# Optimization experiments

Measured on AMD Instinct MI355X. Metric: run time of the kernel, lower is better.

## Reference

```python
import jax, jax.numpy as jnp
import numpy as np

B, S, E, H, F, V = 4, 2048, 1024, 16, 4096, 32000
D = E // H  # head_dim = 64
LN_EPS = 1e-5


def layer_norm(x, g, b):
    mu = jnp.mean(x, axis=-1, keepdims=True)
    var = jnp.mean(jnp.square(x - mu), axis=-1, keepdims=True)
    return (x - mu) * jax.lax.rsqrt(var + LN_EPS) * g + b


def setup_inputs() -> dict:
    key = jax.random.key(0)
    ks = jax.random.split(key, 12)
    s = 0.02
    return {
        "input_ids": jax.random.randint(ks[0], (B, S), 0, V),
        "attention_mask": jnp.ones((B, S), dtype=jnp.int32),
        "emb_table": jax.random.normal(ks[1], (V, E), jnp.float32) * s,
        "Wq": jax.random.normal(ks[2], (E, E), jnp.float32) * s,
        "bq": jnp.zeros((E,), jnp.float32),
        "Wk": jax.random.normal(ks[3], (E, E), jnp.float32) * s,
        "bk": jnp.zeros((E,), jnp.float32),
        "Wv": jax.random.normal(ks[4], (E, E), jnp.float32) * s,
        "bv": jnp.zeros((E,), jnp.float32),
        "Wo": jax.random.normal(ks[5], (E, E), jnp.float32) * s,
        "bo": jnp.zeros((E,), jnp.float32),
        "ln_g": jnp.ones((E,), jnp.float32),
        "ln_b": jnp.zeros((E,), jnp.float32),
        "W1": jax.random.normal(ks[6], (E, F), jnp.float32) * s,
        "b1": jnp.zeros((F,), jnp.float32),
        "W2": jax.random.normal(ks[7], (F, E), jnp.float32) * s,
        "b2": jnp.zeros((E,), jnp.float32),
        "Wp": jax.random.normal(ks[8], (E, 3), jnp.float32) * s,
        "bp": jnp.zeros((3,), jnp.float32),
    }


def reference(input_ids, attention_mask, emb_table, Wq, bq, Wk, bk, Wv, bv,
              Wo, bo, ln_g, ln_b, W1, b1, W2, b2, Wp, bp):
    b, s = input_ids.shape
    x = emb_table[input_ids]                                  # [B,S,E]
    q = (x @ Wq + bq).reshape(b, s, H, D).transpose(0, 2, 1, 3)  # [B,H,S,D]
    k = (x @ Wk + bk).reshape(b, s, H, D).transpose(0, 2, 1, 3)
    v = (x @ Wv + bv).reshape(b, s, H, D).transpose(0, 2, 1, 3)
    scores = jnp.einsum('bhqd,bhkd->bhqk', q, k) / jnp.sqrt(jnp.float32(D))
    mask = attention_mask[:, None, None, :]                   # [B,1,1,S]
    scores = jnp.where(mask == 0, -jnp.inf, scores)
    attn = jax.nn.softmax(scores, axis=-1)
    ctx = jnp.einsum('bhqk,bhkd->bhqd', attn, v)              # [B,H,S,D]
    ctx = ctx.transpose(0, 2, 1, 3).reshape(b, s, E)
    ctx = ctx @ Wo + bo
    h = layer_norm(ctx + x, ln_g, ln_b)
    ff = jax.nn.gelu(h @ W1 + b1, approximate=False) @ W2 + b2
    logits = ff @ Wp + bp                                     # [B,S,3]
    return logits.mean(axis=1)                                # [B,3]
```

## Files before the change

### kernel.cpp

```cpp
#include <hip/hip_runtime.h>
#include <hip/hip_bf16.h>
#include <math.h>

#define BB 4
#define SS 2048
#define EE 1024
#define HH 16
#define DD 64
#define FF 4096

typedef unsigned short u16;
typedef unsigned int u32;
typedef __bf16 bf16x8 __attribute__((ext_vector_type(8)));
typedef float f32x4 __attribute__((ext_vector_type(4)));

static __device__ __forceinline__ float gelu_exact(float v){
  return 0.5f * v * (1.0f + erff(v * 0.70710678118654752f));
}

static __device__ __forceinline__ u16 f2bf(float f){
  union { float f; u32 u; } x; x.f = f;
  u32 r = x.u + 0x7FFFu + ((x.u >> 16) & 1u);
  return (u16)(r >> 16);
}
static __device__ __forceinline__ u16 f2bf_hw(float f){
  union { __bf16 b; u16 u; } c; c.b = (__bf16)f; return c.u;
}
static __device__ __forceinline__ void unpack2(u32 u, float& lo, float& hi){
  union { u32 u; float f; } a, b;
  a.u = u << 16; b.u = u & 0xFFFF0000u;
  lo = a.f; hi = b.f;
}

#define GLOAD_LDS16(g, l) \
  __builtin_amdgcn_global_load_lds((const __attribute__((address_space(1))) void*)(g), \
      (__attribute__((address_space(3))) void*)(l), 16, 0, 0)

static __device__ __forceinline__ void blockbar(){
  asm volatile("" ::: "memory");
  __builtin_amdgcn_s_barrier();
  asm volatile("" ::: "memory");
}

__global__ __launch_bounds__(256) void embed_kernel(const int* __restrict__ ids,
    const float* __restrict__ emb, float* __restrict__ xf, u16* __restrict__ xbf){
  int row = blockIdx.x;
  int id  = ids[row];
  float4 v = ((const float4*)(emb + (size_t)id * EE))[threadIdx.x];
  ((float4*)(xf + (size_t)row * EE))[threadIdx.x] = v;
  ushort4 u; u.x = f2bf(v.x); u.y = f2bf(v.y); u.z = f2bf(v.z); u.w = f2bf(v.w);
  ((ushort4*)(xbf + (size_t)row * EE))[threadIdx.x] = u;
}

__global__ __launch_bounds__(256) void mask_prep(const int* __restrict__ mask,
    float* __restrict__ mbias){
  int i = blockIdx.x * 256 + threadIdx.x;
  mbias[i] = (mask[i] != 0) ? 0.f : -1e30f;
}

__global__ __launch_bounds__(256) void prep_weights(const float* __restrict__ Wq,
    const float* __restrict__ Wk, const float* __restrict__ Wv,
    const float* __restrict__ Wo, const float* __restrict__ W1, u16* __restrict__ WT){
  __shared__ float tile[32][33];
  int bid = blockIdx.x;
  const float* W; u16* dst; int N, n0, k0;
  if (bid < 4096){
    W = W1; dst = WT + (size_t)4 * EE * EE; N = FF;
    n0 = (bid & 127) * 32; k0 = (bid >> 7) * 32;
  } else {
    int idx = bid - 4096;
    int which = idx >> 10, t = idx & 1023;
    W = (which == 0) ? Wq : (which == 1) ? Wk : (which == 2) ? Wv : Wo;
    dst = WT + (size_t)which * EE * EE; N = EE;
    n0 = (t & 31) * 32; k0 = (t >> 5) * 32;
  }
  int tx = threadIdx.x & 31, ty = threadIdx.x >> 5;
  #pragma unroll
  for (int i = 0; i < 4; i++)
    tile[ty + 8*i][tx] = W[(size_t)(k0 + ty + 8*i) * N + n0 + tx];
  __syncthreads();
  #pragma unroll
  for (int i = 0; i < 4; i++)
    dst[(size_t)(n0 + ty + 8*i) * EE + k0 + tx] = f2bf(tile[tx][ty + 8*i]);
}

template<int MODE>
__global__ __launch_bounds__(256) void gemm_mfma(const u16* __restrict__ A,
    const u16* __restrict__ WT, const float* __restrict__ bias,
    const float* __restrict__ biasB, const float* __restrict__ biasC,
    u16* __restrict__ C, float* __restrict__ gsum, int M, int N, int K){
  __shared__ __attribute__((aligned(16))) u16 As[2][128 * 32];
  __shared__ __attribute__((aligned(16))) u16 Bs[2][128 * 32];

  const int tid = threadIdx.x;
  const int l = tid & 63, w = tid >> 6;
  const int lm = l & 15, lq = l >> 4;
  const int wm = (w >> 1) * 64, wn = (w & 1) * 64;

  const int nwg = gridDim.x * gridDim.y;
  const int bid = blockIdx.y * gridDim.x + blockIdx.x;
  const int q8  = nwg >> 3;
  const int lin = (bid & 7) * q8 + (bid >> 3);
  const int bx  = lin % gridDim.x;
  const int by  = lin / gridDim.x;
  const int r0 = by * 128, c0 = bx * 128;

  const int srow0 = w * 32 + (l >> 2);
  const int scol  = (l & 3) * 8;
  const u16* Ab = A  + (size_t)(r0 + srow0) * K + scol;
  const u16* Bb = WT + (size_t)(c0 + srow0) * K + scol;
  const int sbase = (w * 2) * 512;

  f32x4 acc[4][4];
  const f32x4 zero = {0.f, 0.f, 0.f, 0.f};
  #pragma unroll
  for (int mi = 0; mi < 4; mi++)
    #pragma unroll
    for (int ni = 0; ni < 4; ni++) acc[mi][ni] = zero;

  GLOAD_LDS16(Ab,                  &As[0][sbase]);
  GLOAD_LDS16(Ab + (size_t)16 * K, &As[0][sbase + 512]);
  GLOAD_LDS16(Bb,                  &Bs[0][sbase]);
  GLOAD_LDS16(Bb + (size_t)16 * K, &Bs[0][sbase + 512]);
  __syncthreads();

  int p = 0;
  for (int k0 = 0; k0 < K; k0 += 32){
    if (k0 + 32 < K){
      const int pn = p ^ 1;
      GLOAD_LDS16(Ab + k0 + 32,                   &As[pn][sbase]);
      GLOAD_LDS16(Ab + (size_t)16 * K + k0 + 32,  &As[pn][sbase + 512]);
      GLOAD_LDS16(Bb + k0 + 32,                   &Bs[pn][sbase]);
      GLOAD_LDS16(Bb + (size_t)16 * K + k0 + 32,  &Bs[pn][sbase + 512]);
    }
    bf16x8 af[4], bfr[4];
    #pragma unroll
    for (int mi = 0; mi < 4; mi++)
      af[mi] = *(const bf16x8*)&As[p][(wm + mi*16 + lm) * 32 + lq * 8];
    #pragma unroll
    for (int ni = 0; ni < 4; ni++)
      bfr[ni] = *(const bf16x8*)&Bs[p][(wn + ni*16 + lm) * 32 + lq * 8];
    #pragma unroll
    for (int mi = 0; mi < 4; mi++)
      #pragma unroll
      for (int ni = 0; ni < 4; ni++)
        acc[mi][ni] = __builtin_amdgcn_mfma_f32_16x16x32_bf16(af[mi], bfr[ni], acc[mi][ni], 0, 0, 0);
    __syncthreads();
    p ^= 1;
  }

  if constexpr (MODE == 0){
    #pragma unroll
    for (int ni = 0; ni < 4; ni++){
      int col = c0 + wn + ni*16 + lm;
      float bcol = bias[col];
      #pragma unroll
      for (int mi = 0; mi < 4; mi++){
        #pragma unroll
        for (int r = 0; r < 4; r++){
          int row = r0 + wm + mi*16 + lq*4 + r;
          C[(size_t)row * N + col] = f2bf(acc[mi][ni][r] + bcol);
        }
      }
    }
  }
}

template<int MODE>
__global__ __launch_bounds__(512, 2) void gemm256(const u16* __restrict__ A,
    const u16* __restrict__ WT, const float* __restrict__ bias,
    const float* __restrict__ biasB, const float* __restrict__ biasC,
    u16* __restrict__ C, float* __restrict__ gsum, int M, int N, int K){
  __shared__ __attribute__((aligned(16))) u16 As[2 * 256 * 64];
  __shared__ __attribute__((aligned(16))) u16 Bs[2 * 256 * 64];

  const int tid = threadIdx.x;
  const int w = tid >> 6, l = tid & 63;
  const int lm = l & 15, lq = l >> 4;
  const int wm = (w >> 2) * 128, wn = (w & 3) * 64;

  const int nwg = gridDim.x * gridDim.y;
  const int bid = blockIdx.y * gridDim.x + blockIdx.x;
  const int lin = (bid & 7) * (nwg >> 3) + (bid >> 3);
  const int bx = lin % gridDim.x, by = lin / gridDim.x;
  const int r0 = by * 256, c0 = bx * 256;

  const int NT = K >> 6;
  const int arow = w * 8 + (l >> 3);
  const int acol = ((l & 7) ^ (l >> 3)) * 8;
  const u16* Ag = A  + (size_t)(r0 + arow) * K + acol;
  const u16* Bg = WT + (size_t)(c0 + arow) * K + acol;
  const int dstw = w * 512;

#define STG_A(p_, kt_, g_) GLOAD_LDS16(Ag + (size_t)((g_)*64) * K + (kt_)*64, &As[(p_)*16384 + (g_)*4096 + dstw])
#define STG_B(p_, kt_, g_) GLOAD_LDS16(Bg + (size_t)((g_)*64) * K + (kt_)*64, &Bs[(p_)*16384 + (g_)*4096 + dstw])

  const int rsw = (lm & 7) << 3;
#define RD_A(p_, mi_, kk_) (*(const bf16x8*)&As[(p_)*16384 + (wm + (mi_)*16 + lm)*64 + (((kk_)*32 + lq*8) ^ rsw)])
#define RD_B(p_, ni_, kk_) (*(const bf16x8*)&Bs[(p_)*16384 + (wn + (ni_)*16 + lm)*64 + (((kk_)*32 + lq*8) ^ rsw)])

  f32x4 acc[8][4];
  const f32x4 zero = {0.f, 0.f, 0.f, 0.f};
  #pragma unroll
  for (int mi = 0; mi < 8; mi++)
    #pragma unroll
    for (int ni = 0; ni < 4; ni++) acc[mi][ni] = zero;

  #pragma unroll
  for (int g = 0; g < 4; g++){ STG_A(0, 0, g); STG_B(0, 0, g); }
  #pragma unroll
  for (int g = 0; g < 4; g++){ STG_A(1, 1, g); STG_B(1, 1, g); }
  asm volatile("s_waitcnt vmcnt(8)" ::: "memory");
  __builtin_amdgcn_s_barrier();
  asm volatile("" ::: "memory");

  bf16x8 a0[4][2], a1[4][2], b0[2][2], b1[2][2];

  for (int t = 0; t < NT; ++t){
    const int p = t & 1;
    const int s = t + 2;
    const bool st = (s < NT);

    #pragma unroll
    for (int mi = 0; mi < 4; mi++){ a0[mi][0] = RD_A(p, mi, 0); a0[mi][1] = RD_A(p, mi, 1); }
    #pragma unroll
    for (int ni = 0; ni < 2; ni++){ b0[ni][0] = RD_B(p, ni, 0); b0[ni][1] = RD_B(p, ni, 1); }
    blockbar();
    __builtin_amdgcn_s_setprio(1);
    #pragma unroll
    for (int kk = 0; kk < 2; kk++)
      #pragma unroll
      for (int mi = 0; mi < 4; mi++)
        #pragma unroll
        for (int ni = 0; ni < 2; ni++)
          acc[mi][ni] = __builtin_amdgcn_mfma_f32_16x16x32_bf16(a0[mi][kk], b0[ni][kk], acc[mi][ni], 0, 0, 0);
    __builtin_amdgcn_s_setprio(0);
    blockbar();

    #pragma unroll
    for (int ni = 0; ni < 2; ni++){ b1[ni][0] = RD_B(p, ni + 2, 0); b1[ni][1] = RD_B(p, ni + 2, 1); }
    if (st){ STG_A(p, s, 0); STG_A(p, s, 2); }
    blockbar();
    __builtin_amdgcn_s_setprio(1);
    #pragma unroll
    for (int kk = 0; kk < 2; kk++)
      #pragma unroll
      for (int mi = 0; mi < 4; mi++)
        #pragma unroll
        for (int ni = 0; ni < 2; ni++)
          acc[mi][ni + 2] = __builtin_amdgcn_mfma_f32_16x16x32_bf16(a0[mi][kk], b1[ni][kk], acc[mi][ni + 2], 0, 0, 0);
    __builtin_amdgcn_s_setprio(0);
    blockbar();

    #pragma unroll
    for (int mi = 0; mi < 4; mi++){ a1[mi][0] = RD_A(p, mi + 4, 0); a1[mi][1] = RD_A(p, mi + 4, 1); }
    if (st){ STG_B(p, s, 0); STG_B(p, s, 1); }
    blockbar();
    __builtin_amdgcn_s_setprio(1);
    #pragma unroll
    for (int kk = 0; kk < 2; kk++)
      #pragma unroll
      for (int mi = 0; mi < 4; mi++)
        #pragma unroll
        for (int ni = 0; ni < 2; ni++)
          acc[mi + 4][ni] = __builtin_amdgcn_mfma_f32_16x16x32_bf16(a1[mi][kk], b0[ni][kk], acc[mi + 4][ni], 0, 0, 0);
    __builtin_amdgcn_s_setprio(0);
    blockbar();

    if (st){ STG_A(p, s, 1); STG_A(p, s, 3); STG_B(p, s, 2); STG_B(p, s, 3); }
    blockbar();
    __builtin_amdgcn_s_setprio(1);
    #pragma unroll
    for (int kk = 0; kk < 2; kk++)
      #pragma unroll
      for (int mi = 0; mi < 4; mi++)
        #pragma unroll
        for (int ni = 0; ni < 2; ni++)
          acc[mi + 4][ni + 2] = __builtin_amdgcn_mfma_f32_16x16x32_bf16(a1[mi][kk], b1[ni][kk], acc[mi + 4][ni + 2], 0, 0, 0);
    __builtin_amdgcn_s_setprio(0);
    if (t + 1 < NT){
      if (st) asm volatile("s_waitcnt vmcnt(8)" ::: "memory");
      else    asm volatile("s_waitcnt vmcnt(0)" ::: "memory");
      __builtin_amdgcn_s_barrier();
      asm volatile("" ::: "memory");
    }
  }

#undef STG_A
#undef STG_B
#undef RD_A
#undef RD_B

  if constexpr (MODE == 2){
    #pragma unroll
    for (int ni = 0; ni < 4; ni++){
      int col3 = c0 + wn + ni*16 + lm;
      int sel  = col3 >> 10;
      int colm = col3 & 1023;
      const float* bp_ = (sel == 0) ? bias : ((sel == 1) ? biasB : biasC);
      float bcol = bp_[colm];
      u16* dst = C + (size_t)sel * ((size_t)M * 1024);
      #pragma unroll
      for (int mi = 0; mi < 8; mi++){
        #pragma unroll
        for (int r = 0; r < 4; r++){
          int row = r0 + wm + mi*16 + lq*4 + r;
          dst[(size_t)row * 1024 + colm] = f2bf(acc[mi][ni][r] + bcol);
        }
      }
    }
  } else {
    const int batch = (r0 + wm) >> 11;
    #pragma unroll
    for (int ni = 0; ni < 4; ni++){
      int col = c0 + wn + ni*16 + lm;
      float bcol = bias[col];
      float cs = 0.f;
      #pragma unroll
      for (int mi = 0; mi < 8; mi++)
        #pragma unroll
        for (int r = 0; r < 4; r++)
          cs += gelu_exact(acc[mi][ni][r] + bcol);
      cs += __shfl_xor(cs, 16, 64);
      cs += __shfl_xor(cs, 32, 64);
      if (lq == 0) atomicAdd(&gsum[(size_t)batch * N + col], cs);
    }
  }
}

__global__ __launch_bounds__(256, 2) void attn_mfma(const u16* __restrict__ q,
    const u16* __restrict__ k, const u16* __restrict__ v,
    const float* __restrict__ mbias, u16* __restrict__ ctx){
  const int bid = blockIdx.y * gridDim.x + blockIdx.x;
  const int lin = (bid & 7) * 128 + (bid >> 3);
  const int qb  = lin & 15, bh = lin >> 4;
  const int b = bh >> 4, h = bh & 15;
  const int q0 = qb * 128;
  const int tid = threadIdx.x;
  const int w = tid >> 6, l = tid & 63, lm = l & 15, lq = l >> 4;

  __shared__ __attribute__((aligned(16))) u16 smem[128 * 72];
  u16* Kt = smem;
  u16* Vt = smem + 64 * 72;

  bf16x8 aq[2][2];
  #pragma unroll
  for (int mg = 0; mg < 2; mg++){
    const u16* qrow = q + (size_t)(b*SS + q0 + w*32 + mg*16 + lm) * EE + h*DD + lq*8;
    aq[mg][0] = *(const bf16x8*)qrow;
    aq[mg][1] = *(const bf16x8*)(qrow + 32);
  }

  f32x4 occ[2][4];
  const f32x4 zero = {0.f,0.f,0.f,0.f};
  #pragma unroll
  for (int mg = 0; mg < 2; mg++)
    #pragma unroll
    for (int mi = 0; mi < 4; mi++) occ[mg][mi] = zero;
  float l_part[2] = {0.f, 0.f};

  const int kkey = tid >> 2, kc16 = (tid & 3) * 16;
  const u16* kbase = k + (size_t)(b*SS + kkey) * EE + h*DD + kc16;
  const int kp = tid & 31, vd0 = (tid >> 5) * 8;
  const int vslot = ((kp >> 1) & 3) * 8 + ((kp >> 3) & 1) * 4 + (kp & 1) * 2 + (kp >> 4) * 32;
  const u16* vbase0 = v + (size_t)(b*SS + 2*kp) * EE + h*DD + vd0;
  const u16* vbase1 = vbase0 + EE;

  uint4 kr0 = *(const uint4*)(kbase);
  uint4 kr1 = *(const uint4*)(kbase + 8);
  uint4 vr0 = *(const uint4*)(vbase0);
  uint4 vr1 = *(const uint4*)(vbase1);

  const float SCALE_LOG2E = 0.125f * 1.4426950408889634f;
  const float* mrow = mbias + (size_t)b * SS;

  for (int t0 = 0; t0 < SS; t0 += 64){
    *(uint4*)&Kt[kkey*72 + kc16]     = kr0;
    *(uint4*)&Kt[kkey*72 + kc16 + 8] = kr1;
    {
      union { uint4 u; u16 s[8]; } va, vb;
      va.u = vr0; vb.u = vr1;
      #pragma unroll
      for (int i = 0; i < 8; i++){
        u32 pk = (u32)va.s[i] | ((u32)vb.s[i] << 16);
        *(u32*)&Vt[(vd0 + i)*72 + vslot] = pk;
      }
    }
    __syncthreads();

    if (t0 + 64 < SS){
      kr0 = *(const uint4*)(kbase + (size_t)(t0 + 64) * EE);
      kr1 = *(const uint4*)(kbase + (size_t)(t0 + 64) * EE + 8);
      vr0 = *(const uint4*)(vbase0 + (size_t)(t0 + 64) * EE);
      vr1 = *(const uint4*)(vbase1 + (size_t)(t0 + 64) * EE);
    }

    f32x4 mt[4];
    #pragma unroll
    for (int ni = 0; ni < 4; ni++)
      mt[ni] = *(const f32x4*)&mrow[t0 + ni*16 + lq*4];

    bf16x8 pb[2][2];
    #pragma unroll
    for (int mg = 0; mg < 2; mg++){
      float lp = 0.f;
      #pragma unroll
      for (int h2 = 0; h2 < 2; h2++){
        u32 pk_[2][2];
        #pragma unroll
        for (int np = 0; np < 2; np++){
          int ni = h2*2 + np;
          bf16x8 kf0 = *(const bf16x8*)&Kt[(ni*16 + lm)*72 + lq*8];
          bf16x8 kf1 = *(const bf16x8*)&Kt[(ni*16 + lm)*72 + 32 + lq*8];
          f32x4 sc = zero;
          __builtin_amdgcn_s_setprio(1);
          sc = __builtin_amdgcn_mfma_f32_16x16x32_bf16(kf0, aq[mg][0], sc, 0, 0, 0);
          sc = __builtin_amdgcn_mfma_f32_16x16x32_bf16(kf1, aq[mg][1], sc, 0, 0, 0);
          __builtin_amdgcn_s_setprio(0);
          float p[4];
          #pragma unroll
          for (int r = 0; r < 4; r++){
            float s = fminf(fmaf(sc[r], SCALE_LOG2E, mt[ni][r]), 80.f);
            p[r] = __builtin_amdgcn_exp2f(s);
            lp += p[r];
          }
          pk_[np][0] = (u32)f2bf_hw(p[0]) | ((u32)f2bf_hw(p[1]) << 16);
          pk_[np][1] = (u32)f2bf_hw(p[2]) | ((u32)f2bf_hw(p[3]) << 16);
        }
        union { u32 u[4]; bf16x8 v; } pu;
        pu.u[0] = pk_[0][0];
        pu.u[1] = pk_[0][1];
        pu.u[2] = pk_[1][0];
        pu.u[3] = pk_[1][1];
        pb[mg][h2] = pu.v;
      }
      l_part[mg] += lp;
    }

    __builtin_amdgcn_s_setprio(1);
    #pragma unroll
    for (int mi = 0; mi < 4; mi++){
      bf16x8 vb0 = *(const bf16x8*)&Vt[(mi*16 + lm)*72 + lq*8];
      bf16x8 vb1 = *(const bf16x8*)&Vt[(mi*16 + lm)*72 + 32 + lq*8];
      #pragma unroll
      for (int mg = 0; mg < 2; mg++){
        occ[mg][mi] = __builtin_amdgcn_mfma_f32_16x16x32_bf16(vb0, pb[mg][0], occ[mg][mi], 0, 0, 0);
        occ[mg][mi] = __builtin_amdgcn_mfma_f32_16x16x32_bf16(vb1, pb[mg][1], occ[mg][mi], 0, 0, 0);
      }
    }
    __builtin_amdgcn_s_setprio(0);
    __syncthreads();
  }

  #pragma unroll
  for (int mg = 0; mg < 2; mg++){
    float s = l_part[mg];
    s += __shfl_xor(s, 16, 64);
    s += __shfl_xor(s, 32, 64);
    float inv = 1.f / s;
    #pragma unroll
    for (int mi = 0; mi < 4; mi++){
      ushort4 o;
      o.x = f2bf(occ[mg][mi][0] * inv);
      o.y = f2bf(occ[mg][mi][1] * inv);
      o.z = f2bf(occ[mg][mi][2] * inv);
      o.w = f2bf(occ[mg][mi][3] * inv);
      *(ushort4*)&smem[(w*32 + mg*16 + lm)*72 + mi*16 + lq*4] = o;
    }
  }
  __syncthreads();
  {
    const int row = tid >> 1, half = tid & 1;
    u16* dst = ctx + (size_t)(b*SS + q0 + row) * EE + h*DD + half*32;
    const u16* src = &smem[row*72 + half*32];
    #pragma unroll
    for (int jj = 0; jj < 4; jj++)
      *(uint4*)(dst + jj*8) = *(const uint4*)(src + jj*8);
  }
}

__global__ __launch_bounds__(256) void ln_kernel(const u16* __restrict__ c2,
    const float* __restrict__ x, const float* __restrict__ g,
    const float* __restrict__ bta, u16* __restrict__ h){
  int row = blockIdx.x, tid = threadIdx.x;
  uint2 cu = ((const uint2*)(c2 + (size_t)row * EE))[tid];
  float c0,c1,c2f,c3;
  unpack2(cu.x, c0, c1); unpack2(cu.y, c2f, c3);
  float4 xv = ((const float4*)(x + (size_t)row * EE))[tid];
  float4 y = make_float4(c0+xv.x, c1+xv.y, c2f+xv.z, c3+xv.w);
  float s  = y.x + y.y + y.z + y.w;
  float ss = y.x*y.x + y.y*y.y + y.z*y.z + y.w*y.w;
  #pragma unroll
  for (int off=32; off; off>>=1){
    s  += __shfl_xor(s,  off, 64);
    ss += __shfl_xor(ss, off, 64);
  }
  __shared__ float rs[4], rss[4];
  int w = tid >> 6;
  if ((tid & 63) == 0){ rs[w] = s; rss[w] = ss; }
  __syncthreads();
  float tot  = rs[0]+rs[1]+rs[2]+rs[3];
  float tots = rss[0]+rss[1]+rss[2]+rss[3];
  float mu  = tot  * (1.f/EE);
  float var = tots * (1.f/EE) - mu*mu;
  float inv = rsqrtf(var + 1e-5f);
  float4 gv = ((const float4*)g)[tid];
  float4 bv = ((const float4*)bta)[tid];
  ushort4 ou;
  ou.x = f2bf((y.x-mu)*inv*gv.x + bv.x);
  ou.y = f2bf((y.y-mu)*inv*gv.y + bv.y);
  ou.z = f2bf((y.z-mu)*inv*gv.z + bv.z);
  ou.w = f2bf((y.w-mu)*inv*gv.w + bv.w);
  ((ushort4*)(h + (size_t)row * EE))[tid] = ou;
}

__global__ __launch_bounds__(256) void w2wp_kernel(const float* __restrict__ W2,
    const float* __restrict__ Wp, float* __restrict__ W2Wp){
  int f0 = blockIdx.x * 8;
  int tid = threadIdx.x;
  int e0 = tid * 4;
  float wp[4][3];
  #pragma unroll
  for (int t = 0; t < 4; t++)
    #pragma unroll
    for (int j = 0; j < 3; j++) wp[t][j] = Wp[(e0 + t)*3 + j];
  __shared__ float red[3][4];
  for (int i = 0; i < 8; i++){
    int f = f0 + i;
    float4 wv = ((const float4*)(W2 + (size_t)f * EE))[tid];
    float w4[4] = {wv.x, wv.y, wv.z, wv.w};
    float p[3] = {0.f, 0.f, 0.f};
    #pragma unroll
    for (int t = 0; t < 4; t++)
      #pragma unroll
      for (int j = 0; j < 3; j++) p[j] += w4[t] * wp[t][j];
    #pragma unroll
    for (int j = 0; j < 3; j++){
      float sj = p[j];
      #pragma unroll
      for (int off = 32; off; off >>= 1) sj += __shfl_xor(sj, off, 64);
      if ((tid & 63) == 0) red[j][tid >> 6] = sj;
    }
    __syncthreads();
    if (tid < 3) W2Wp[f*3 + tid] = red[tid][0] + red[tid][1] + red[tid][2] + red[tid][3];
    __syncthreads();
  }
}

__global__ __launch_bounds__(256) void out_final(const float* __restrict__ gsum,
    const float* __restrict__ W2Wp, const float* __restrict__ b2,
    const float* __restrict__ Wp, const float* __restrict__ bp, float* __restrict__ out){
  int tid = threadIdx.x;
  float part[4][3];
  #pragma unroll
  for (int b = 0; b < 4; b++)
    #pragma unroll
    for (int j = 0; j < 3; j++) part[b][j] = 0.f;
  for (int f = tid; f < FF; f += 256){
    float w0 = W2Wp[f*3], w1 = W2Wp[f*3+1], w2v = W2Wp[f*3+2];
    #pragma unroll
    for (int b = 0; b < 4; b++){
      float g = gsum[b*FF + f] * (1.f/SS);
      part[b][0] += g * w0; part[b][1] += g * w1; part[b][2] += g * w2v;
    }
  }
  float bb[3] = {0.f, 0.f, 0.f};
  for (int e = tid; e < EE; e += 256){
    float bv = b2[e];
    bb[0] += bv * Wp[e*3]; bb[1] += bv * Wp[e*3+1]; bb[2] += bv * Wp[e*3+2];
  }
  __shared__ float red[15][4];
  int lane = tid & 63, w = tid >> 6;
  #pragma unroll
  for (int b = 0; b < 4; b++)
    #pragma unroll
    for (int j = 0; j < 3; j++){
      float s = part[b][j];
      #pragma unroll
      for (int off = 32; off; off >>= 1) s += __shfl_xor(s, off, 64);
      if (lane == 0) red[b*3 + j][w] = s;
    }
  #pragma unroll
  for (int j = 0; j < 3; j++){
    float s = bb[j];
    #pragma unroll
    for (int off = 32; off; off >>= 1) s += __shfl_xor(s, off, 64);
    if (lane == 0) red[12 + j][w] = s;
  }
  __syncthreads();
  if (tid < 12){
    int j = tid % 3;
    float s  = red[tid][0] + red[tid][1] + red[tid][2] + red[tid][3];
    float bj = red[12+j][0] + red[12+j][1] + red[12+j][2] + red[12+j][3];
    out[tid] = s + bj + bp[j];
  }
}

extern "C" void kernel_launch(void* const* d_in, const int* in_sizes, int n_in,
                              void* d_out, int out_size, void* d_ws, size_t ws_size,
                              hipStream_t stream) {
  const int M = BB * SS;
  const int* ids  = (const int*)d_in[0];
  const int* mask = (const int*)d_in[1];
  const float* emb = (const float*)d_in[2];
  const float* Wq = (const float*)d_in[3];  const float* bq = (const float*)d_in[4];
  const float* Wk = (const float*)d_in[5];  const float* bk = (const float*)d_in[6];
  const float* Wv = (const float*)d_in[7];  const float* bv = (const float*)d_in[8];
  const float* Wo = (const float*)d_in[9];  const float* bo = (const float*)d_in[10];
  const float* lg = (const float*)d_in[11]; const float* lb = (const float*)d_in[12];
  const float* W1 = (const float*)d_in[13]; const float* b1 = (const float*)d_in[14];
  const float* W2 = (const float*)d_in[15]; const float* b2 = (const float*)d_in[16];
  const float* Wp = (const float*)d_in[17]; const float* bp = (const float*)d_in[18];

  char* base = (char*)d_ws;
  const size_t SLOTF = (size_t)M * EE;
  float* xf   = (float*)base;
  u16*  xbf   = (u16*)(base + SLOTF*4);
  u16*  qbf   = (u16*)(base + SLOTF*6);
  u16*  kbf   = (u16*)(base + SLOTF*8);
  u16*  vbf   = (u16*)(base + SLOTF*10);
  u16*  ctxbf = (u16*)(base + SLOTF*12);
  u16*  c2bf  = qbf;
  u16*  hbf   = kbf;
  u16*  WqT   = (u16*)(base + SLOTF*14);
  u16*  W1T   = WqT + (size_t)4*EE*EE;
  float* gsum = (float*)(W1T + (size_t)FF*EE);
  float* w2wp = gsum + BB*FF;
  float* mbias = w2wp + FF*3;

  hipMemsetAsync(gsum, 0, BB*FF*sizeof(float), stream);

  embed_kernel<<<M, 256, 0, stream>>>(ids, emb, xf, xbf);
  mask_prep<<<BB*SS/256, 256, 0, stream>>>(mask, mbias);

  prep_weights<<<8192, 256, 0, stream>>>(Wq, Wk, Wv, Wo, W1, WqT);
  w2wp_kernel<<<FF/8, 256, 0, stream>>>(W2, Wp, w2wp);

  gemm256<2><<<dim3(3*EE/256, M/256), 512, 0, stream>>>(
      xbf, WqT, bq, bk, bv, qbf, nullptr, M, EE, EE);

  attn_mfma<<<dim3(SS/128, BB*HH), 256, 0, stream>>>(qbf, kbf, vbf, mbias, ctxbf);

  gemm_mfma<0><<<dim3(EE/128, M/128), 256, 0, stream>>>(
      ctxbf, WqT + (size_t)3*EE*EE, bo, nullptr, nullptr, c2bf, nullptr, M, EE, EE);

  ln_kernel<<<M, 256, 0, stream>>>(c2bf, xf, lg, lb, hbf);

  gemm256<1><<<dim3(FF/256, M/256), 512, 0, stream>>>(
      hbf, W1T, b1, nullptr, nullptr, nullptr, gsum, M, FF, EE);

  out_final<<<1, 256, 0, stream>>>(gsum, w2wp, b2, Wp, bp, (float*)d_out);
}
```

Measured before the change: 593.5 us.

## Stream K tiles directly to LDS with double-buffered swizzled layout in attention

The attention kernel now loads K tiles with direct global-to-LDS loads (GLOAD_LDS16) into two ping-pong buffers with an XOR swizzle instead of padded rows staged through registers. This removes the register round trip and the LDS store instructions for K, and lets the next tile's K load overlap with the current compute. It also drops the fminf clamp before exp2, which saves an instruction per score but removes overflow protection. Shared memory grows from 128*72 to 12800 elements, which could affect occupancy.

```diff
diff --git a/kernel.cpp b/kernel.cpp
--- a/kernel.cpp
+++ b/kernel.cpp
@@ -339,9 +339,10 @@
   const int tid = threadIdx.x;
   const int w = tid >> 6, l = tid & 63, lm = l & 15, lq = l >> 4;
 
-  __shared__ __attribute__((aligned(16))) u16 smem[128 * 72];
-  u16* Kt = smem;
-  u16* Vt = smem + 64 * 72;
+  __shared__ __attribute__((aligned(16))) u16 smem[12800];
+  u16* Kt0 = smem;
+  u16* Kt1 = smem + 4096;
+  u16* Vt  = smem + 8192;
 
   bf16x8 aq[2][2];
   #pragma unroll
@@ -359,24 +360,29 @@
     for (int mi = 0; mi < 4; mi++) occ[mg][mi] = zero;
   float l_part[2] = {0.f, 0.f};
 
-  const int kkey = tid >> 2, kc16 = (tid & 3) * 16;
-  const u16* kbase = k + (size_t)(b*SS + kkey) * EE + h*DD + kc16;
+  const int krow = (l >> 3);
+  const int kchk = ((l & 7) ^ (krow & 7)) * 8;
+  const u16* kg0 = k + (size_t)(b*SS + w*16 + krow) * EE + h*DD + kchk;
+  const u16* kg1 = kg0 + (size_t)8 * EE;
+  const int kd0 = w*1024;
+  const int kd1 = w*1024 + 512;
+  const int rswl = (lm & 7) << 3;
+
   const int kp = tid & 31, vd0 = (tid >> 5) * 8;
   const int vslot = ((kp >> 1) & 3) * 8 + ((kp >> 3) & 1) * 4 + (kp & 1) * 2 + (kp >> 4) * 32;
   const u16* vbase0 = v + (size_t)(b*SS + 2*kp) * EE + h*DD + vd0;
   const u16* vbase1 = vbase0 + EE;
 
-  uint4 kr0 = *(const uint4*)(kbase);
-  uint4 kr1 = *(const uint4*)(kbase + 8);
+  GLOAD_LDS16(kg0, &Kt0[kd0]);
+  GLOAD_LDS16(kg1, &Kt0[kd1]);
   uint4 vr0 = *(const uint4*)(vbase0);
   uint4 vr1 = *(const uint4*)(vbase1);
 
   const float SCALE_LOG2E = 0.125f * 1.4426950408889634f;
   const float* mrow = mbias + (size_t)b * SS;
 
+  int p = 0;
   for (int t0 = 0; t0 < SS; t0 += 64){
-    *(uint4*)&Kt[kkey*72 + kc16]     = kr0;
-    *(uint4*)&Kt[kkey*72 + kc16 + 8] = kr1;
     {
       union { uint4 u; u16 s[8]; } va, vb;
       va.u = vr0; vb.u = vr1;
@@ -389,11 +395,13 @@
     __syncthreads();
 
     if (t0 + 64 < SS){
-      kr0 = *(const uint4*)(kbase + (size_t)(t0 + 64) * EE);
-      kr1 = *(const uint4*)(kbase + (size_t)(t0 + 64) * EE + 8);
+      u16* Ktn = p ? Kt0 : Kt1;
+      GLOAD_LDS16(kg0 + (size_t)(t0 + 64) * EE, &Ktn[kd0]);
+      GLOAD_LDS16(kg1 + (size_t)(t0 + 64) * EE, &Ktn[kd1]);
       vr0 = *(const uint4*)(vbase0 + (size_t)(t0 + 64) * EE);
       vr1 = *(const uint4*)(vbase1 + (size_t)(t0 + 64) * EE);
     }
+    const u16* Ktp = p ? Kt1 : Kt0;
 
     f32x4 mt[4];
     #pragma unroll
@@ -410,22 +418,22 @@
         #pragma unroll
         for (int np = 0; np < 2; np++){
           int ni = h2*2 + np;
-          bf16x8 kf0 = *(const bf16x8*)&Kt[(ni*16 + lm)*72 + lq*8];
-          bf16x8 kf1 = *(const bf16x8*)&Kt[(ni*16 + lm)*72 + 32 + lq*8];
+          bf16x8 kf0 = *(const bf16x8*)&Ktp[(ni*16 + lm)*64 + ((lq*8) ^ rswl)];
+          bf16x8 kf1 = *(const bf16x8*)&Ktp[(ni*16 + lm)*64 + ((32 + lq*8) ^ rswl)];
           f32x4 sc = zero;
           __builtin_amdgcn_s_setprio(1);
           sc = __builtin_amdgcn_mfma_f32_16x16x32_bf16(kf0, aq[mg][0], sc, 0, 0, 0);
           sc = __builtin_amdgcn_mfma_f32_16x16x32_bf16(kf1, aq[mg][1], sc, 0, 0, 0);
           __builtin_amdgcn_s_setprio(0);
-          float p[4];
+          float pr[4];
           #pragma unroll
           for (int r = 0; r < 4; r++){
-            float s = fminf(fmaf(sc[r], SCALE_LOG2E, mt[ni][r]), 80.f);
-            p[r] = __builtin_amdgcn_exp2f(s);
-            lp += p[r];
+            float s = fmaf(sc[r], SCALE_LOG2E, mt[ni][r]);
+            pr[r] = __builtin_amdgcn_exp2f(s);
+            lp += pr[r];
           }
-          pk_[np][0] = (u32)f2bf_hw(p[0]) | ((u32)f2bf_hw(p[1]) << 16);
-          pk_[np][1] = (u32)f2bf_hw(p[2]) | ((u32)f2bf_hw(p[3]) << 16);
+          pk_[np][0] = (u32)f2bf_hw(pr[0]) | ((u32)f2bf_hw(pr[1]) << 16);
+          pk_[np][1] = (u32)f2bf_hw(pr[2]) | ((u32)f2bf_hw(pr[3]) << 16);
         }
         union { u32 u[4]; bf16x8 v; } pu;
         pu.u[0] = pk_[0][0];
@@ -450,6 +458,7 @@
     }
     __builtin_amdgcn_s_setprio(0);
     __syncthreads();
+    p ^= 1;
   }
 
   #pragma unroll
```

After: 583.7 us. No clear change (-1.7%).
